# Kernel tuning notes

Measured on AMD Instinct MI355X. Metric: run time of the kernel, lower is better.

The kernel has to match this reference:

```python
import jax, jax.numpy as jnp
import numpy as np

G, L, H = 8, 16, 768  # num_global_heads, num_local_heads, hidden_dim
D = H // G            # head_size = 96
B, N = 16, 512


def setup_inputs() -> dict:
    key = jax.random.key(0)
    ks = jax.random.split(key, 10)
    inp = {
        "x": jax.random.normal(ks[0], (B, N, H), dtype=jnp.float32),
        "encoding_bias": jax.random.normal(ks[1], (B, N, N), dtype=jnp.float32),
        # noise injected into global attention scores (randn_like(g_k))
        "eps": jax.random.normal(ks[2], (B, G, N, N), dtype=jnp.float32),
        # params: torch Linear stored here as (in, out) so y = x @ W
        "Wq": jax.random.normal(ks[3], (H, H), dtype=jnp.float32) / np.sqrt(H),
        "Wk": jax.random.normal(ks[4], (H, H), dtype=jnp.float32) / np.sqrt(H),
        "Wv": jax.random.normal(ks[5], (H, L * D), dtype=jnp.float32) / np.sqrt(H),
        "bv": jax.random.normal(ks[6], (L * D,), dtype=jnp.float32) * 0.01,
        "sigma": 0.1 * jnp.ones((G,), dtype=jnp.float32),
        "p": jax.random.normal(ks[7], (G, L), dtype=jnp.float32),
        "Wout": jax.random.normal(ks[8], (L * D, H), dtype=jnp.float32) / np.sqrt(L * D),
    }
    return inp


def mish(x):
    return x * jnp.tanh(jax.nn.softplus(x))


def reference(x, encoding_bias, eps, Wq, Wk, Wv, bv, sigma, p, Wout):
    b, n, h = x.shape
    g, l = p.shape
    d = h // g
    scale = h ** (-0.5)
    bias = encoding_bias[:, None, :, :]  # (b,1,n,n)

    q = (x @ Wq).reshape(b, n, g, d)
    k = (x @ Wk).reshape(b, n, g, d)
    v = (x @ Wv + bv).reshape(b, n, l, d)

    g_k = jnp.einsum('bngd,bmgd->bgnm', q, k)            # global QK^T
    pad_mask = jnp.all(g_k == 0, axis=-1)                # (b,g,n) padded rows
    a = g_k + (sigma ** 2)[None, :, None, None] * eps    # noise injection
    a = jnp.where(pad_mask[..., None], 0.0, a)

    a = jnp.einsum('bgnm,gl->blnm', a, p)                # head admixture
    pad_mask2 = jnp.all(a == 0, axis=-1)                 # (b,l,n)
    a = jnp.where(pad_mask2[..., None], -jnp.inf, mish(a))

    a = a * scale + bias
    a = jax.nn.softmax(a, axis=-1)
    a = jnp.nan_to_num(a)                                # all -inf rows -> 0

    o = jnp.einsum('blnm,bmld->bnld', a, v)              # (b,n,l,d); dropout = eval identity
    return o.reshape(b, n, l * d) @ Wout
```

## Files before the change

### kernel.cpp

```cpp
#include <hip/hip_runtime.h>
#include <stdint.h>
#include <stddef.h>

typedef __attribute__((ext_vector_type(8))) short bf16x8;
typedef __attribute__((ext_vector_type(4))) short s16x4;
typedef __attribute__((ext_vector_type(4))) float f32x4;

__device__ __forceinline__ short f2bf(float x) {
  uint32_t u = __builtin_bit_cast(uint32_t, x);
  u += 0x7fffu + ((u >> 16) & 1u);
  return (short)(u >> 16);
}

__device__ __forceinline__ void gload16(const short* g, short* l) {
  __builtin_amdgcn_global_load_lds(
      (const __attribute__((address_space(1))) void*)g,
      (__attribute__((address_space(3))) void*)l, 16, 0, 0);
}

#define PB 16
#define PN 512
#define PH 768
#define PG 8
#define PD 96
#define PL 16
#define PLD 1536
#define PC 3072

__global__ void transpose_bf16_k(const float* __restrict__ src, short* __restrict__ dst,
                                 int R, int C) {
  __shared__ float tile[32][33];
  int c0 = blockIdx.x * 32, r0 = blockIdx.y * 32;
  int tx = threadIdx.x;
  int ty = threadIdx.y;
  for (int i = 0; i < 4; i++) {
    int r = r0 + ty + i * 8;
    tile[ty + i * 8][tx] = src[(size_t)r * C + c0 + tx];
  }
  __syncthreads();
  for (int i = 0; i < 4; i++) {
    int c = c0 + ty + i * 8;
    dst[(size_t)c * R + r0 + tx] = f2bf(tile[tx][ty + i * 8]);
  }
}

__global__ __launch_bounds__(256) void convert_bf16_k(const float* __restrict__ src,
                                                      short* __restrict__ dst) {
  int i = (blockIdx.x * 256 + threadIdx.x) * 4;
  float4 v = *(const float4*)(src + i);
  s16x4 o = { f2bf(v.x), f2bf(v.y), f2bf(v.z), f2bf(v.w) };
  *(s16x4*)(dst + i) = o;
}

__global__ __launch_bounds__(256) void gemm_qkv_k(
    const short* __restrict__ Xb, const short* __restrict__ Wt,
    const float* __restrict__ bv, short* __restrict__ Cb) {
  __shared__ short As[128 * 32];
  __shared__ short Bs[128 * 32];
  int n0 = blockIdx.x * 128;
  int m0 = blockIdx.y * 128;
  int tid = threadIdx.x;
  int wave = tid >> 6, lane = tid & 63, quad = lane >> 4, l16 = lane & 15;
  int wm = wave & 1, wn = wave >> 1;

  f32x4 acc[4][4] = {};

  for (int k0 = 0; k0 < PH; k0 += 32) {
#pragma unroll
    for (int t = 0; t < 2; t++) {
      int rb = (wave * 2 + t) * 16;
      gload16(Xb + (size_t)(m0 + rb + (lane >> 2)) * PH + k0 + (lane & 3) * 8,
              &As[rb * 32]);
      gload16(Wt + (size_t)(n0 + rb + (lane >> 2)) * PH + k0 + (lane & 3) * 8,
              &Bs[rb * 32]);
    }
    __syncthreads();
    bf16x8 af[4], bfv[4];
#pragma unroll
    for (int i = 0; i < 4; i++)
      af[i] = *(bf16x8*)&As[(wm * 64 + i * 16 + l16) * 32 + quad * 8];
#pragma unroll
    for (int j = 0; j < 4; j++)
      bfv[j] = *(bf16x8*)&Bs[(wn * 64 + j * 16 + l16) * 32 + quad * 8];
#pragma unroll
    for (int i = 0; i < 4; i++)
#pragma unroll
      for (int j = 0; j < 4; j++)
        acc[i][j] = __builtin_amdgcn_mfma_f32_16x16x32_bf16(af[i], bfv[j], acc[i][j], 0, 0, 0);
    __syncthreads();
  }

  bool isv = (n0 >= 2 * PH);
  float bvr[4] = {0.f, 0.f, 0.f, 0.f};
  if (isv)
#pragma unroll
    for (int j = 0; j < 4; j++)
      bvr[j] = bv[n0 + wn * 64 + j * 16 + l16 - 2 * PH];

#pragma unroll
  for (int i = 0; i < 4; i++) {
    int rowb = m0 + wm * 64 + i * 16 + quad * 4;
#pragma unroll
    for (int j = 0; j < 4; j++) {
      int col = n0 + wn * 64 + j * 16 + l16;
#pragma unroll
      for (int r = 0; r < 4; r++)
        Cb[(size_t)(rowb + r) * PC + col] = f2bf(acc[i][j][r] + bvr[j]);
    }
  }
}

__global__ __launch_bounds__(256) void vtrans2_k(const short* __restrict__ Cb,
                                                 short* __restrict__ vbt) {
  __shared__ short tile[32][36];
  int b = blockIdx.z;
  int ld0 = blockIdx.y * 32;
  int n0 = blockIdx.x * 32;
  int t = threadIdx.x;
  int r = t >> 3, c = (t & 7) * 4;
  *(uint2*)&tile[r][c] =
      *(const uint2*)(Cb + ((size_t)(b * PN) + n0 + r) * PC + 2 * PH + ld0 + c);
  __syncthreads();
  s16x4 o = { tile[c + 0][r], tile[c + 1][r], tile[c + 2][r], tile[c + 3][r] };
  *(s16x4*)(vbt + ((size_t)(b * PLD) + ld0 + r) * PN + n0 + c) = o;
}

#define SB_STR 68
#define PB_STR 72
__global__ __launch_bounds__(256, 2) void fused_attn_k(
    const short* __restrict__ Cb, const float* __restrict__ eps,
    const float* __restrict__ ebias, const float* __restrict__ sigma,
    const float* __restrict__ p, const short* __restrict__ vbt,
    short* __restrict__ ob) {
  __shared__ __align__(16) char ubuf[16 * PB_STR * PL * 2];
  __shared__ float pLs[PG][PL];
  __shared__ float sg2s[PG];
  float* sb = (float*)ubuf;
  short* pb = (short*)ubuf;

  int n0 = blockIdx.x * 16;
  int b = blockIdx.y;
  int tid = threadIdx.x;
  int wave = tid >> 6, lane = tid & 63, quad = lane >> 4, l16 = lane & 15;

  if (tid < PG * PL) pLs[tid >> 4][tid & 15] = p[tid];
  if (tid < PG) { float s = sigma[tid]; sg2s[tid] = s * s; }
  __syncthreads();
  float sg2r[PG];
#pragma unroll
  for (int g = 0; g < PG; g++) sg2r[g] = sg2s[g];

  const float scale = 0.03608439182435161f;

  bf16x8 aq[2][3];
#pragma unroll
  for (int gg = 0; gg < 2; gg++) {
    int g = wave * 2 + gg;
    const short* qg = Cb + ((size_t)(b * PN) + n0 + l16) * PC + g * PD;
#pragma unroll
    for (int ks = 0; ks < 3; ks++)
      aq[gg][ks] = *(const bf16x8*)(qg + ks * 32 + quad * 8);
  }

  bf16x8 onesf;
#pragma unroll
  for (int j = 0; j < 8; j++) onesf[j] = (short)0x3F80;

  f32x4 oacc[4][6] = {};
  f32x4 sacc[4] = {};

  for (int mt = 0; mt < 8; mt++) {
    int m0 = mt * 64;
    float er[4][PG];
    float br[4];
#pragma unroll
    for (int s = 0; s < 4; s++) {
      int n = wave + 4 * s;
#pragma unroll
      for (int g = 0; g < PG; g++)
        er[s][g] = eps[((size_t)(b * PG + g) * PN + n0 + n) * PN + m0 + lane];
      br[s] = ebias[((size_t)b * PN + n0 + n) * PN + m0 + lane];
    }
#pragma unroll
    for (int gg = 0; gg < 2; gg++) {
      int g = wave * 2 + gg;
      const short* kg = Cb + ((size_t)(b * PN) + m0) * PC + PH + g * PD;
#pragma unroll
      for (int ms = 0; ms < 4; ms++) {
        f32x4 acc = {};
#pragma unroll
        for (int ks = 0; ks < 3; ks++) {
          bf16x8 bk = *(const bf16x8*)(kg + (size_t)(ms * 16 + l16) * PC + ks * 32 + quad * 8);
          acc = __builtin_amdgcn_mfma_f32_16x16x32_bf16(aq[gg][ks], bk, acc, 0, 0, 0);
        }
#pragma unroll
        for (int r = 0; r < 4; r++)
          sb[g * (16 * SB_STR) + (quad * 4 + r) * SB_STR + ms * 16 + l16] = acc[r];
      }
    }
    __syncthreads();
    float sv[4][PG];
#pragma unroll
    for (int s = 0; s < 4; s++) {
      int n = wave + 4 * s;
#pragma unroll
      for (int g = 0; g < PG; g++)
        sv[s][g] = sb[g * (16 * SB_STR) + n * SB_STR + lane] + sg2r[g] * er[s][g];
    }
    __syncthreads();
    for (int l = 0; l < PL; l++) {
      float a0 = 0.f, a1 = 0.f, a2 = 0.f, a3 = 0.f;
#pragma unroll
      for (int g = 0; g < PG; g++) {
        float pv = pLs[g][l];
        a0 += sv[0][g] * pv; a1 += sv[1][g] * pv;
        a2 += sv[2][g] * pv; a3 += sv[3][g] * pv;
      }
      float as[4] = {a0, a1, a2, a3};
#pragma unroll
      for (int s = 0; s < 4; s++) {
        float a = as[s];
        float ex = __expf(a);
        float t = 1.f + ex;
        float r2 = t * t;
        float mi = (a > 20.f) ? a : a * (r2 - 1.f) * __builtin_amdgcn_rcpf(r2 + 1.f);
        float e = __expf(mi * scale + br[s]);
        pb[l * (16 * PB_STR) + (wave + 4 * s) * PB_STR + lane] = f2bf(e);
      }
    }
    __syncthreads();
#pragma unroll
    for (int li = 0; li < 4; li++) {
      int l = wave * 4 + li;
      bf16x8 af0 = *(bf16x8*)&pb[l * (16 * PB_STR) + l16 * PB_STR + 0 + quad * 8];
      bf16x8 af1 = *(bf16x8*)&pb[l * (16 * PB_STR) + l16 * PB_STR + 32 + quad * 8];
      const short* vb = vbt + ((size_t)(b * PL + l) * PD) * PN + m0;
#pragma unroll
      for (int dt = 0; dt < 6; dt++) {
        bf16x8 b0 = *(const bf16x8*)(vb + (size_t)(dt * 16 + l16) * PN + quad * 8);
        bf16x8 b1 = *(const bf16x8*)(vb + (size_t)(dt * 16 + l16) * PN + 32 + quad * 8);
        oacc[li][dt] = __builtin_amdgcn_mfma_f32_16x16x32_bf16(af0, b0, oacc[li][dt], 0, 0, 0);
        oacc[li][dt] = __builtin_amdgcn_mfma_f32_16x16x32_bf16(af1, b1, oacc[li][dt], 0, 0, 0);
      }
      sacc[li] = __builtin_amdgcn_mfma_f32_16x16x32_bf16(af0, onesf, sacc[li], 0, 0, 0);
      sacc[li] = __builtin_amdgcn_mfma_f32_16x16x32_bf16(af1, onesf, sacc[li], 0, 0, 0);
    }
    __syncthreads();
  }

#pragma unroll
  for (int li = 0; li < 4; li++) {
    int l = wave * 4 + li;
#pragma unroll
    for (int r = 0; r < 4; r++) {
      int n = quad * 4 + r;
      float inv = __builtin_amdgcn_rcpf(sacc[li][r]);
#pragma unroll
      for (int dt = 0; dt < 6; dt++) {
        float o = oacc[li][dt][r] * inv;
        ob[((size_t)(b * PN) + n0 + n) * PLD + l * PD + dt * 16 + l16] = f2bf(o);
      }
    }
  }
}

__global__ __launch_bounds__(256) void gemm_out_k(
    const short* __restrict__ A, const short* __restrict__ Bt,
    float* __restrict__ out) {
  __shared__ short As[128 * 32];
  __shared__ short Bs[128 * 32];
  int n0 = blockIdx.x * 128;
  int m0 = blockIdx.y * 128;
  int tid = threadIdx.x;
  int wave = tid >> 6, lane = tid & 63, quad = lane >> 4, l16 = lane & 15;
  int wm = wave & 1, wn = wave >> 1;
  f32x4 acc[4][4] = {};
  for (int k0 = 0; k0 < PLD; k0 += 32) {
#pragma unroll
    for (int t = 0; t < 2; t++) {
      int rb = (wave * 2 + t) * 16;
      gload16(A + (size_t)(m0 + rb + (lane >> 2)) * PLD + k0 + (lane & 3) * 8,
              &As[rb * 32]);
      gload16(Bt + (size_t)(n0 + rb + (lane >> 2)) * PLD + k0 + (lane & 3) * 8,
              &Bs[rb * 32]);
    }
    __syncthreads();
    bf16x8 af[4], bfv[4];
#pragma unroll
    for (int i = 0; i < 4; i++)
      af[i] = *(bf16x8*)&As[(wm * 64 + i * 16 + l16) * 32 + quad * 8];
#pragma unroll
    for (int j = 0; j < 4; j++)
      bfv[j] = *(bf16x8*)&Bs[(wn * 64 + j * 16 + l16) * 32 + quad * 8];
#pragma unroll
    for (int i = 0; i < 4; i++)
#pragma unroll
      for (int j = 0; j < 4; j++)
        acc[i][j] = __builtin_amdgcn_mfma_f32_16x16x32_bf16(af[i], bfv[j], acc[i][j], 0, 0, 0);
    __syncthreads();
  }
#pragma unroll
  for (int i = 0; i < 4; i++) {
    int rowb = m0 + wm * 64 + i * 16 + quad * 4;
#pragma unroll
    for (int j = 0; j < 4; j++) {
      int col = n0 + wn * 64 + j * 16 + l16;
#pragma unroll
      for (int r = 0; r < 4; r++)
        out[(size_t)(rowb + r) * PH + col] = acc[i][j][r];
    }
  }
}

extern "C" void kernel_launch(void* const* d_in, const int* in_sizes, int n_in,
                              void* d_out, int out_size, void* d_ws, size_t ws_size,
                              hipStream_t stream) {
  (void)in_sizes; (void)n_in; (void)out_size; (void)ws_size;
  const float* x     = (const float*)d_in[0];
  const float* ebias = (const float*)d_in[1];
  const float* eps   = (const float*)d_in[2];
  const float* Wq    = (const float*)d_in[3];
  const float* Wk    = (const float*)d_in[4];
  const float* Wv    = (const float*)d_in[5];
  const float* bv    = (const float*)d_in[6];
  const float* sigma = (const float*)d_in[7];
  const float* p     = (const float*)d_in[8];
  const float* Wout  = (const float*)d_in[9];
  float* out = (float*)d_out;

  char* ws = (char*)d_ws;
  short* xb     = (short*)(ws + 0);
  short* wqkv_t = (short*)(ws + 12582912);
  short* wout_t = (short*)(ws + 17301504);
  short* Cb     = (short*)(ws + 19660800);
  short* vbt    = (short*)(ws + 69992448);
  short* ob     = (short*)(ws + 95158272);

  dim3 tb(32, 8);
  transpose_bf16_k<<<dim3(24, 24), tb, 0, stream>>>(Wq, wqkv_t, PH, PH);
  transpose_bf16_k<<<dim3(24, 24), tb, 0, stream>>>(Wk, wqkv_t + 768 * 768, PH, PH);
  transpose_bf16_k<<<dim3(48, 24), tb, 0, stream>>>(Wv, wqkv_t + 1536 * 768, PH, PLD);
  transpose_bf16_k<<<dim3(24, 48), tb, 0, stream>>>(Wout, wout_t, PLD, PH);
  convert_bf16_k<<<dim3(6144), 256, 0, stream>>>(x, xb);

  gemm_qkv_k<<<dim3(24, 64), 256, 0, stream>>>(xb, wqkv_t, bv, Cb);
  vtrans2_k<<<dim3(16, 48, 16), 256, 0, stream>>>(Cb, vbt);
  fused_attn_k<<<dim3(32, 16), 256, 0, stream>>>(Cb, eps, ebias, sigma, p, vbt, ob);
  gemm_out_k<<<dim3(6, 64), 256, 0, stream>>>(ob, wout_t, out);
}
```

Before: 536.2 us.

## Split shared buffers, prefetch next eps/bias tile, drop a barrier, pair math

Splits the aliased shared buffer into separate score and probability arrays so one barrier per tile can be removed. The eps and encoding-bias loads for the next key tile are issued before the current tile's mish/exp work, so global-load latency overlaps with compute. The admixture accumulation is regrouped into float2 pairs, which may allow packed FMA. Shared memory use rises, which may lower occupancy at two blocks per CU, and the prefetch keeps more values live in registers.

```diff
diff --git a/kernel.cpp b/kernel.cpp
--- a/kernel.cpp
+++ b/kernel.cpp
@@ -132,11 +132,10 @@
     const float* __restrict__ ebias, const float* __restrict__ sigma,
     const float* __restrict__ p, const short* __restrict__ vbt,
     short* __restrict__ ob) {
-  __shared__ __align__(16) char ubuf[16 * PB_STR * PL * 2];
+  __shared__ __align__(16) float sb[PG][16 * SB_STR];
+  __shared__ __align__(16) short pb[PL][16 * PB_STR];
   __shared__ float pLs[PG][PL];
   __shared__ float sg2s[PG];
-  float* sb = (float*)ubuf;
-  short* pb = (short*)ubuf;
 
   int n0 = blockIdx.x * 16;
   int b = blockIdx.y;
@@ -169,18 +168,19 @@
   f32x4 oacc[4][6] = {};
   f32x4 sacc[4] = {};
 
+  float er[4][PG];
+  float br[4];
+#pragma unroll
+  for (int s = 0; s < 4; s++) {
+    int n = wave + 4 * s;
+#pragma unroll
+    for (int g = 0; g < PG; g++)
+      er[s][g] = eps[((size_t)(b * PG + g) * PN + n0 + n) * PN + lane];
+    br[s] = ebias[((size_t)b * PN + n0 + n) * PN + lane];
+  }
+
   for (int mt = 0; mt < 8; mt++) {
     int m0 = mt * 64;
-    float er[4][PG];
-    float br[4];
-#pragma unroll
-    for (int s = 0; s < 4; s++) {
-      int n = wave + 4 * s;
-#pragma unroll
-      for (int g = 0; g < PG; g++)
-        er[s][g] = eps[((size_t)(b * PG + g) * PN + n0 + n) * PN + m0 + lane];
-      br[s] = ebias[((size_t)b * PN + n0 + n) * PN + m0 + lane];
-    }
 #pragma unroll
     for (int gg = 0; gg < 2; gg++) {
       int g = wave * 2 + gg;
@@ -195,45 +195,60 @@
         }
 #pragma unroll
         for (int r = 0; r < 4; r++)
-          sb[g * (16 * SB_STR) + (quad * 4 + r) * SB_STR + ms * 16 + l16] = acc[r];
-      }
-    }
-    __syncthreads();
-    float sv[4][PG];
-#pragma unroll
-    for (int s = 0; s < 4; s++) {
-      int n = wave + 4 * s;
-#pragma unroll
-      for (int g = 0; g < PG; g++)
-        sv[s][g] = sb[g * (16 * SB_STR) + n * SB_STR + lane] + sg2r[g] * er[s][g];
-    }
-    __syncthreads();
+          sb[g][(quad * 4 + r) * SB_STR + ms * 16 + l16] = acc[r];
+      }
+    }
+    __syncthreads();
+    float2 sv[2][PG];
+#pragma unroll
+    for (int sp = 0; sp < 2; sp++) {
+      int na = wave + 4 * (2 * sp), nb_ = wave + 4 * (2 * sp + 1);
+#pragma unroll
+      for (int g = 0; g < PG; g++) {
+        sv[sp][g].x = sb[g][na * SB_STR + lane] + sg2r[g] * er[2 * sp][g];
+        sv[sp][g].y = sb[g][nb_ * SB_STR + lane] + sg2r[g] * er[2 * sp + 1][g];
+      }
+    }
+    float bias2[2][2] = {{br[0], br[1]}, {br[2], br[3]}};
+    {
+      int m0n = (mt < 7) ? (m0 + 64) : m0;
+#pragma unroll
+      for (int s = 0; s < 4; s++) {
+        int n = wave + 4 * s;
+#pragma unroll
+        for (int g = 0; g < PG; g++)
+          er[s][g] = eps[((size_t)(b * PG + g) * PN + n0 + n) * PN + m0n + lane];
+        br[s] = ebias[((size_t)b * PN + n0 + n) * PN + m0n + lane];
+      }
+    }
     for (int l = 0; l < PL; l++) {
-      float a0 = 0.f, a1 = 0.f, a2 = 0.f, a3 = 0.f;
+      float2 a2[2] = {{0.f, 0.f}, {0.f, 0.f}};
 #pragma unroll
       for (int g = 0; g < PG; g++) {
         float pv = pLs[g][l];
-        a0 += sv[0][g] * pv; a1 += sv[1][g] * pv;
-        a2 += sv[2][g] * pv; a3 += sv[3][g] * pv;
-      }
-      float as[4] = {a0, a1, a2, a3};
-#pragma unroll
-      for (int s = 0; s < 4; s++) {
-        float a = as[s];
-        float ex = __expf(a);
-        float t = 1.f + ex;
-        float r2 = t * t;
-        float mi = (a > 20.f) ? a : a * (r2 - 1.f) * __builtin_amdgcn_rcpf(r2 + 1.f);
-        float e = __expf(mi * scale + br[s]);
-        pb[l * (16 * PB_STR) + (wave + 4 * s) * PB_STR + lane] = f2bf(e);
+        a2[0].x += sv[0][g].x * pv; a2[0].y += sv[0][g].y * pv;
+        a2[1].x += sv[1][g].x * pv; a2[1].y += sv[1][g].y * pv;
+      }
+#pragma unroll
+      for (int sp = 0; sp < 2; sp++) {
+#pragma unroll
+        for (int h = 0; h < 2; h++) {
+          float a = h ? a2[sp].y : a2[sp].x;
+          float ex = __expf(a);
+          float t = 1.f + ex;
+          float r2 = t * t;
+          float mi = (a > 20.f) ? a : a * (r2 - 1.f) * __builtin_amdgcn_rcpf(r2 + 1.f);
+          float e = __expf(mi * scale + bias2[sp][h]);
+          pb[l][(wave + 4 * (2 * sp + h)) * PB_STR + lane] = f2bf(e);
+        }
       }
     }
     __syncthreads();
 #pragma unroll
     for (int li = 0; li < 4; li++) {
       int l = wave * 4 + li;
-      bf16x8 af0 = *(bf16x8*)&pb[l * (16 * PB_STR) + l16 * PB_STR + 0 + quad * 8];
-      bf16x8 af1 = *(bf16x8*)&pb[l * (16 * PB_STR) + l16 * PB_STR + 32 + quad * 8];
+      bf16x8 af0 = *(bf16x8*)&pb[l][l16 * PB_STR + 0 + quad * 8];
+      bf16x8 af1 = *(bf16x8*)&pb[l][l16 * PB_STR + 32 + quad * 8];
       const short* vb = vbt + ((size_t)(b * PL + l) * PD) * PN + m0;
 #pragma unroll
       for (int dt = 0; dt < 6; dt++) {
@@ -245,7 +260,6 @@
       sacc[li] = __builtin_amdgcn_mfma_f32_16x16x32_bf16(af0, onesf, sacc[li], 0, 0, 0);
       sacc[li] = __builtin_amdgcn_mfma_f32_16x16x32_bf16(af1, onesf, sacc[li], 0, 0, 0);
     }
-    __syncthreads();
   }
 
 #pragma unroll
```

After: 570.8 us. 1.06x slower.
